# Performance work log

Measured on AMD Instinct MI355X. Metric: run time of the kernel, lower is better.

## Reference

```python
import jax, jax.numpy as jnp
import numpy as np

N = 50000
E = 800000
D = 128

def setup_inputs() -> dict:
    key = jax.random.key(0)
    ks = jax.random.split(key, 10)
    s = 1.0 / np.sqrt(D)
    return {
        "hidden": jax.random.normal(ks[0], (N, D), dtype=jnp.float32),
        "edge_index": jax.random.randint(ks[1], (2, E), 0, N, dtype=jnp.int64),
        "edge_attr": jax.random.uniform(ks[2], (E, 1), dtype=jnp.float32),
        # edge_encoder: Linear(1, D)
        "We": jax.random.uniform(ks[3], (1, D), minval=-1.0, maxval=1.0, dtype=jnp.float32),
        "be": jax.random.uniform(ks[4], (D,), minval=-1.0, maxval=1.0, dtype=jnp.float32),
        # mlp: Linear(D,D) -> ReLU -> Linear(D,D); weights stored [in,out]
        "W1": jax.random.uniform(ks[5], (D, D), minval=-s, maxval=s, dtype=jnp.float32),
        "b1": jax.random.uniform(ks[6], (D,), minval=-s, maxval=s, dtype=jnp.float32),
        "W2": jax.random.uniform(ks[7], (D, D), minval=-s, maxval=s, dtype=jnp.float32),
        "b2": jax.random.uniform(ks[8], (D,), minval=-s, maxval=s, dtype=jnp.float32),
        "eps": jnp.zeros((1,), dtype=jnp.float32),
    }

def reference(hidden, edge_index, edge_attr, We, be, W1, b1, W2, b2, eps):
    # NOTE: original forward computes relu(hidden) but discards it, passing
    # raw `hidden` into the conv; replicated faithfully.
    src, dst = edge_index[0], edge_index[1]
    edge_emb = edge_attr @ We + be                      # [E, D]
    msg = jax.nn.relu(hidden[src] + edge_emb)           # gather + message
    summed = jax.ops.segment_sum(msg, dst, num_segments=N)           # [N, D]
    cnt = jax.ops.segment_sum(jnp.ones((E,), hidden.dtype), dst, num_segments=N)
    aggr = summed / jnp.maximum(cnt, 1.0)[:, None]      # scatter-mean
    h = (1.0 + eps[0]) * hidden + aggr
    h = jax.nn.relu(h @ W1 + b1)
    out = h @ W2 + b2
    return out
```

## Files before the change

### kernel.cpp

```cpp
#include <hip/hip_runtime.h>

static constexpr int N_NODES = 50000;
static constexpr int D = 128;
static constexpr int E_EDGES = 800000;
static constexpr int SLOTS = 48;
static constexpr int TILES = N_NODES / 16;
static constexpr int NROWS = N_NODES + 8;

static constexpr int BKW  = 192;
static constexpr int NB   = (N_NODES + BKW - 1) / BKW;
static constexpr int CAP  = 4096;
static constexpr int EPB  = 4096;
static constexpr int ABIN = (E_EDGES + EPB - 1) / EPB;
static constexpr int ACVT = (E_EDGES + 511) / 512;
static constexpr int AWPR = 9;

using half8   = __attribute__((ext_vector_type(8))) _Float16;
using half2v  = __attribute__((ext_vector_type(2))) _Float16;
using floatx4 = __attribute__((ext_vector_type(4))) float;

__global__ __launch_bounds__(512) void bin_coarse(
    const float* __restrict__ hidden,
    const int* __restrict__ edge_index,
    const float* __restrict__ edge_attr,
    const float* __restrict__ W1, const float* __restrict__ W2,
    _Float16* __restrict__ hidden16,
    _Float16* __restrict__ W1f, _Float16* __restrict__ W2f,
    int* __restrict__ bucketFill, int2* __restrict__ coarse)
{
    const int t = threadIdx.x;
    const int b = blockIdx.x;

    if (b >= ABIN + ACVT) {
        int p = (b - ABIN - ACVT) * 512 + t;
        if (p >= 4096) {
            int q = p - 4096;
            if (q < 16) {
                half8 o;
                #pragma unroll
                for (int j = 0; j < 8; ++j) o[j] = (_Float16)(-100.0f);
                ((half8*)(hidden16 + (size_t)N_NODES * D))[q] = o;
            }
            return;
        }
        int lane  = p & 63;
        int ntile = (p >> 6) & 7;
        int kstep = (p >> 9) & 3;
        int mat   = p >> 11;
        const float* W = mat ? W2 : W1;
        _Float16*   Wf = mat ? W2f : W1f;
        int n     = ntile * 16 + (lane & 15);
        int kbase = kstep * 32 + (lane >> 4) * 8;
        _Float16* dst = Wf + ((size_t)((kstep * 8 + ntile) * 64 + lane)) * 8;
        #pragma unroll
        for (int j = 0; j < 8; ++j)
            dst[j] = (_Float16)W[(size_t)(kbase + j) * D + n];
        return;
    }
    if (b >= ABIN) {
        int e = (b - ABIN) * 512 + t;
        if (e < N_NODES * D / 8) {
            float4 v0 = *((const float4*)hidden + 2 * (size_t)e);
            float4 v1 = *((const float4*)hidden + 2 * (size_t)e + 1);
            half8 o;
            o[0] = (_Float16)v0.x; o[1] = (_Float16)v0.y;
            o[2] = (_Float16)v0.z; o[3] = (_Float16)v0.w;
            o[4] = (_Float16)v1.x; o[5] = (_Float16)v1.y;
            o[6] = (_Float16)v1.z; o[7] = (_Float16)v1.w;
            ((half8*)hidden16)[e] = o;
        }
        return;
    }

    __shared__ int lcnt[NB];
    __shared__ int lbase[NB];
    if (t < NB) lcnt[t] = 0;
    __syncthreads();

    const int ebase = b * EPB;
    int src[8], bk[8], dl[8], rank[8];
    float at[8];
    #pragma unroll
    for (int k = 0; k < 8; ++k) {
        int e = ebase + k * 512 + t;
        bool v = e < E_EDGES;
        int d  = v ? edge_index[E_EDGES + e] : 0;
        src[k] = v ? edge_index[e] : 0;
        at[k]  = v ? edge_attr[e] : 0.f;
        bk[k]  = (int)((unsigned)d / (unsigned)BKW);
        dl[k]  = d - bk[k] * BKW;
        rank[k] = v ? 0 : -1;
    }
    #pragma unroll
    for (int k = 0; k < 8; ++k)
        if (rank[k] >= 0)
            rank[k] = atomicAdd(&lcnt[bk[k]], 1);
    __syncthreads();

    if (t < NB) {
        int c = lcnt[t];
        lbase[t] = (c > 0) ? atomicAdd(&bucketFill[t], c) : 0;
    }
    __syncthreads();

    #pragma unroll
    for (int k = 0; k < 8; ++k) {
        if (rank[k] >= 0) {
            int idx = lbase[bk[k]] + rank[k];
            if (idx < CAP)
                coarse[(size_t)bk[k] * CAP + idx] =
                    make_int2(src[k] | (dl[k] << 16), __float_as_int(at[k]));
        }
    }
}

__global__ __launch_bounds__(512) void bin_fine(
    const int2* __restrict__ coarse,
    const int* __restrict__ bucketFill,
    int* __restrict__ counts, int2* __restrict__ csr)
{
    __shared__ int2 tile[BKW * SLOTS];
    __shared__ int  lcnt[BKW];
    const int t  = threadIdx.x;
    const int b  = blockIdx.x;
    const int n0 = b * BKW;
    const int nn = min(N_NODES - n0, BKW);

    int4* tz = (int4*)tile;
    for (int i = t; i < BKW * SLOTS / 2; i += 512)
        tz[i] = make_int4(N_NODES, 0, N_NODES, 0);
    if (t < BKW) lcnt[t] = 0;
    __syncthreads();

    const int cnt = min(__builtin_amdgcn_readfirstlane(bucketFill[b]), CAP);
    const int2* seg = coarse + (size_t)b * CAP;
    for (int r = t; r < cnt; r += 512) {
        int2 rec = seg[r];
        int d   = (rec.x >> 16) & 0xff;
        int pos = atomicAdd(&lcnt[d], 1);
        if (pos < SLOTS)
            tile[d * SLOTS + pos] = make_int2(rec.x & 0xffff, rec.y);
    }
    __syncthreads();

    int4* gout = (int4*)(csr + (size_t)n0 * SLOTS);
    const int4* tin = (const int4*)tile;
    const int nq = nn * SLOTS / 2;
    for (int i = t; i < nq; i += 512)
        gout[i] = tin[i];
    if (t < nn) counts[n0 + t] = lcnt[t];
}

__global__ __launch_bounds__(512) void fused_gather_mlp(
    const _Float16* __restrict__ hidden16,
    const int2* __restrict__ csr,
    const int* __restrict__ counts,
    const float* __restrict__ We, const float* __restrict__ be,
    const float* __restrict__ eps,
    const _Float16* __restrict__ W1f, const float* __restrict__ b1,
    const _Float16* __restrict__ W2f, const float* __restrict__ b2,
    float* __restrict__ out)
{
    __shared__ _Float16 hA[16 * 136];
    __shared__ _Float16 tB[16 * 136];
    const int tid  = threadIdx.x;
    const int wave = tid >> 6;
    const int lane = tid & 63;
    const int node0 = blockIdx.x * 16;
    const int d0 = lane << 1;

    const float2 wv = *(const float2*)(We + d0);
    const float2 bv = *(const float2*)(be + d0);
    const float onePlusEps = 1.0f + eps[0];

    const int nbase = node0 + __builtin_amdgcn_readfirstlane(wave << 1);
    const int2 c2 = *(const int2*)(counts + nbase);
    int dg[2];
    dg[0] = c2.x; dg[1] = c2.y;

    int m_[2];
    const int2* ep[2];
    #pragma unroll
    for (int i = 0; i < 2; ++i) {
        m_[i] = min(dg[i], SLOTS);
        ep[i] = csr + (size_t)(nbase + i) * SLOTS;
    }
    float a0[2] = {0.f, 0.f};
    float a1[2] = {0.f, 0.f};
    const int mmax = max(m_[0], m_[1]);

    #pragma unroll 1
    for (int j = 0; j < mmax; j += 8) {
        #pragma unroll
        for (int u = 0; u < 8; ++u) {
            #pragma unroll
            for (int i = 0; i < 2; ++i) {
                int2 rec = ep[i][j + u];
                int   src = rec.x;
                float at  = __int_as_float(rec.y);
                half2v hp = *(const half2v*)(hidden16 + ((size_t)src << 7) + d0);
                a0[i] += fmaxf((float)hp.x + __builtin_fmaf(at, wv.x, bv.x), 0.f);
                a1[i] += fmaxf((float)hp.y + __builtin_fmaf(at, wv.y, bv.y), 0.f);
            }
        }
    }

    #pragma unroll
    for (int i = 0; i < 2; ++i) {
        const int row = (nbase - node0) + i;
        const float rin = 1.0f / fmaxf((float)dg[i], 1.0f);
        half2v hidp = *(const half2v*)(hidden16 + (size_t)(nbase + i) * D + d0);
        half2v o;
        o.x = (_Float16)(onePlusEps * (float)hidp.x + a0[i] * rin);
        o.y = (_Float16)(onePlusEps * (float)hidp.y + a1[i] * rin);
        *(half2v*)&hA[row * 136 + d0] = o;
    }
    __syncthreads();

    const int ln16 = lane & 15;
    const int quad = lane >> 4;
    const int nt   = wave;

    half8 a[4];
    #pragma unroll
    for (int ks = 0; ks < 4; ++ks)
        a[ks] = *(const half8*)&hA[ln16 * 136 + ks * 32 + quad * 8];

    floatx4 acc;
    {
        float bb = b1[nt * 16 + ln16];
        acc = (floatx4){bb, bb, bb, bb};
        #pragma unroll
        for (int ks = 0; ks < 4; ++ks) {
            half8 b = *(const half8*)(W1f + ((size_t)((ks * 8 + nt) * 64 + lane)) * 8);
            acc = __builtin_amdgcn_mfma_f32_16x16x32_f16(a[ks], b, acc, 0, 0, 0);
        }
    }
    #pragma unroll
    for (int r = 0; r < 4; ++r)
        tB[(quad * 4 + r) * 136 + nt * 16 + ln16] = (_Float16)fmaxf(acc[r], 0.f);
    __syncthreads();

    #pragma unroll
    for (int ks = 0; ks < 4; ++ks)
        a[ks] = *(const half8*)&tB[ln16 * 136 + ks * 32 + quad * 8];

    {
        float bb = b2[nt * 16 + ln16];
        acc = (floatx4){bb, bb, bb, bb};
        #pragma unroll
        for (int ks = 0; ks < 4; ++ks) {
            half8 b = *(const half8*)(W2f + ((size_t)((ks * 8 + nt) * 64 + lane)) * 8);
            acc = __builtin_amdgcn_mfma_f32_16x16x32_f16(a[ks], b, acc, 0, 0, 0);
        }
    }
    #pragma unroll
    for (int r = 0; r < 4; ++r)
        __builtin_nontemporal_store(
            acc[r], &out[(size_t)(node0 + quad * 4 + r) * D + nt * 16 + ln16]);
}

extern "C" void kernel_launch(void* const* d_in, const int* in_sizes, int n_in,
                              void* d_out, int out_size, void* d_ws, size_t ws_size,
                              hipStream_t stream) {
    const float* hidden     = (const float*)d_in[0];
    const int*   edge_index = (const int*)d_in[1];
    const float* edge_attr  = (const float*)d_in[2];
    const float* We         = (const float*)d_in[3];
    const float* be         = (const float*)d_in[4];
    const float* W1         = (const float*)d_in[5];
    const float* b1         = (const float*)d_in[6];
    const float* W2         = (const float*)d_in[7];
    const float* b2         = (const float*)d_in[8];
    const float* eps        = (const float*)d_in[9];
    float* out = (float*)d_out;

    _Float16* hidden16   = (_Float16*)d_ws;
    _Float16* W1f        = hidden16 + (size_t)NROWS * D;
    _Float16* W2f        = W1f + (size_t)D * D;
    int*      counts     = (int*)(W2f + (size_t)D * D);
    int2*     csr        = (int2*)(counts + N_NODES);
    int*      bucketFill = (int*)(csr + (size_t)N_NODES * SLOTS);
    int2*     coarse     = (int2*)(bucketFill + 272);

    hipMemsetAsync(bucketFill, 0, NB * sizeof(int), stream);

    bin_coarse<<<ABIN + ACVT + AWPR, 512, 0, stream>>>(
        hidden, edge_index, edge_attr, W1, W2, hidden16, W1f, W2f,
        bucketFill, coarse);

    bin_fine<<<NB, 512, 0, stream>>>(coarse, bucketFill, counts, csr);

    fused_gather_mlp<<<TILES, 512, 0, stream>>>(
        hidden16, csr, counts, We, be, eps, W1f, b1, W2f, b2, out);
}
```

Baseline: 148.6 us.

## Sort nodes by degree within each bucket to balance wave gather work

bin_fine now builds a small degree histogram for each 192-node bucket and writes a per-bucket permutation that orders nodes by in-degree. The fused gather/MLP kernel processes nodes in permuted order, so the two nodes sharing a wave have similar degree. This cuts the wasted iterations caused by looping to the larger of the two degrees. In exchange it adds a permutation array, an extra block-wide sync, indirect counts and csr lookups, and scattered output row stores.

Measured after the change: 153.8 us. +3.5%, slower.

```diff
diff --git a/kernel.cpp b/kernel.cpp
--- a/kernel.cpp
+++ b/kernel.cpp
@@ -117,10 +117,13 @@
 __global__ __launch_bounds__(512) void bin_fine(
     const int2* __restrict__ coarse,
     const int* __restrict__ bucketFill,
-    int* __restrict__ counts, int2* __restrict__ csr)
+    int* __restrict__ counts, int* __restrict__ perm,
+    int2* __restrict__ csr)
 {
     __shared__ int2 tile[BKW * SLOTS];
     __shared__ int  lcnt[BKW];
+    __shared__ int  h49[SLOTS + 1];
+    __shared__ int  cur[SLOTS + 1];
     const int t  = threadIdx.x;
     const int b  = blockIdx.x;
     const int n0 = b * BKW;
@@ -130,6 +133,7 @@
     for (int i = t; i < BKW * SLOTS / 2; i += 512)
         tz[i] = make_int4(N_NODES, 0, N_NODES, 0);
     if (t < BKW) lcnt[t] = 0;
+    if (t < SLOTS + 1) h49[t] = 0;
     __syncthreads();
 
     const int cnt = min(__builtin_amdgcn_readfirstlane(bucketFill[b]), CAP);
@@ -148,19 +152,36 @@
     const int nq = nn * SLOTS / 2;
     for (int i = t; i < nq; i += 512)
         gout[i] = tin[i];
-    if (t < nn) counts[n0 + t] = lcnt[t];
+    if (t < nn) {
+        counts[n0 + t] = lcnt[t];
+        atomicAdd(&h49[min(lcnt[t], SLOTS)], 1);
+    }
+    __syncthreads();
+
+    if (t == 0) {
+        int o = 0;
+        for (int d = 0; d <= SLOTS; ++d) { cur[d] = o; o += h49[d]; }
+    }
+    __syncthreads();
+
+    if (t < nn) {
+        int pos = atomicAdd(&cur[min(lcnt[t], SLOTS)], 1);
+        perm[n0 + pos] = n0 + t;
+    }
 }
 
 __global__ __launch_bounds__(512) void fused_gather_mlp(
     const _Float16* __restrict__ hidden16,
     const int2* __restrict__ csr,
     const int* __restrict__ counts,
+    const int* __restrict__ perm,
     const float* __restrict__ We, const float* __restrict__ be,
     const float* __restrict__ eps,
     const _Float16* __restrict__ W1f, const float* __restrict__ b1,
     const _Float16* __restrict__ W2f, const float* __restrict__ b2,
     float* __restrict__ out)
 {
+    __shared__ int pr[16];
     __shared__ _Float16 hA[16 * 136];
     __shared__ _Float16 tB[16 * 136];
     const int tid  = threadIdx.x;
@@ -173,18 +194,21 @@
     const float2 bv = *(const float2*)(be + d0);
     const float onePlusEps = 1.0f + eps[0];
 
-    const int nbase = node0 + __builtin_amdgcn_readfirstlane(wave << 1);
-    const int2 c2 = *(const int2*)(counts + nbase);
+    if (tid < 16) pr[tid] = perm[node0 + tid];
+    __syncthreads();
+
+    const int nA = __builtin_amdgcn_readfirstlane(pr[wave << 1]);
+    const int nB = __builtin_amdgcn_readfirstlane(pr[(wave << 1) + 1]);
     int dg[2];
-    dg[0] = c2.x; dg[1] = c2.y;
+    dg[0] = counts[nA];
+    dg[1] = counts[nB];
 
     int m_[2];
     const int2* ep[2];
-    #pragma unroll
-    for (int i = 0; i < 2; ++i) {
-        m_[i] = min(dg[i], SLOTS);
-        ep[i] = csr + (size_t)(nbase + i) * SLOTS;
-    }
+    ep[0] = csr + (size_t)nA * SLOTS;
+    ep[1] = csr + (size_t)nB * SLOTS;
+    m_[0] = min(dg[0], SLOTS);
+    m_[1] = min(dg[1], SLOTS);
     float a0[2] = {0.f, 0.f};
     float a1[2] = {0.f, 0.f};
     const int mmax = max(m_[0], m_[1]);
@@ -207,9 +231,10 @@
 
     #pragma unroll
     for (int i = 0; i < 2; ++i) {
-        const int row = (nbase - node0) + i;
+        const int node = i ? nB : nA;
+        const int row  = (wave << 1) + i;
         const float rin = 1.0f / fmaxf((float)dg[i], 1.0f);
-        half2v hidp = *(const half2v*)(hidden16 + (size_t)(nbase + i) * D + d0);
+        half2v hidp = *(const half2v*)(hidden16 + (size_t)node * D + d0);
         half2v o;
         o.x = (_Float16)(onePlusEps * (float)hidp.x + a0[i] * rin);
         o.y = (_Float16)(onePlusEps * (float)hidp.y + a1[i] * rin);
@@ -255,9 +280,11 @@
         }
     }
     #pragma unroll
-    for (int r = 0; r < 4; ++r)
+    for (int r = 0; r < 4; ++r) {
+        const int prow = pr[quad * 4 + r];
         __builtin_nontemporal_store(
-            acc[r], &out[(size_t)(node0 + quad * 4 + r) * D + nt * 16 + ln16]);
+            acc[r], &out[(size_t)prow * D + nt * 16 + ln16]);
+    }
 }
 
 extern "C" void kernel_launch(void* const* d_in, const int* in_sizes, int n_in,
@@ -279,7 +306,8 @@
     _Float16* W1f        = hidden16 + (size_t)NROWS * D;
     _Float16* W2f        = W1f + (size_t)D * D;
     int*      counts     = (int*)(W2f + (size_t)D * D);
-    int2*     csr        = (int2*)(counts + N_NODES);
+    int*      perm       = counts + N_NODES;
+    int2*     csr        = (int2*)(perm + N_NODES);
     int*      bucketFill = (int*)(csr + (size_t)N_NODES * SLOTS);
     int2*     coarse     = (int2*)(bucketFill + 272);
 
@@ -289,8 +317,8 @@
         hidden, edge_index, edge_attr, W1, W2, hidden16, W1f, W2f,
         bucketFill, coarse);
 
-    bin_fine<<<NB, 512, 0, stream>>>(coarse, bucketFill, counts, csr);
+    bin_fine<<<NB, 512, 0, stream>>>(coarse, bucketFill, counts, perm, csr);
 
     fused_gather_mlp<<<TILES, 512, 0, stream>>>(
-        hidden16, csr, counts, We, be, eps, W1f, b1, W2f, b2, out);
+        hidden16, csr, counts, perm, We, be, eps, W1f, b1, W2f, b2, out);
 }
```
